# Performance work log

Measured on AMD Instinct MI355X. Metric: run time of the kernel, lower is better.

The kernel has to match this reference:

```python
import jax, jax.numpy as jnp
import numpy as np
import math

B, L, C_IN = 256, 128, 75
D_EMB = 128      # DataEmbedding d_model
D_MODEL = 126    # encoder d_model (= L-2 after ODConv valid conv k=3)
H = 6
D_HEAD = D_MODEL // H  # 21
D_FF = 2048
FACTOR = 5
K_NUM = 4        # ODConv kernel_num (default)
ATT_CH = 16      # max(int(128*0.0625), 16)
EPS = 1e-5


def _ln(x, g, b):
    m = x.mean(-1, keepdims=True)
    v = ((x - m) ** 2).mean(-1, keepdims=True)
    return (x - m) * jax.lax.rsqrt(v + EPS) * g + b


def _bn_eval(x, g, b):
    # eval-mode BatchNorm, running_mean=0 running_var=1
    return x * (g / np.sqrt(1.0 + EPS)) + b


def _conv1d(x, w, b=None):
    out = jax.lax.conv_general_dilated(x, w, (1,), 'VALID',
                                       dimension_numbers=('NCH', 'OIH', 'NCH'))
    if b is not None:
        out = out + b[None, :, None]
    return out


def _pos_embed(n, d):
    pos = np.arange(n)[:, None].astype(np.float32)
    div = np.exp(np.arange(0, d, 2).astype(np.float32) * (-math.log(10000.0) / d))
    pe = np.zeros((n, d), np.float32)
    pe[:, 0::2] = np.sin(pos * div)
    pe[:, 1::2] = np.cos(pos * div)
    return jnp.asarray(pe)


def _prob_attention(Q, K, V, key):
    # Informer ProbAttention, mask_flag=False. Q,K,V: [B,H,Lq,D]
    b, h, lq, d = Q.shape
    lk = K.shape[2]
    u_keys = min(FACTOR * int(np.ceil(np.log(lk))), lk)
    n_top = min(FACTOR * int(np.ceil(np.log(lq))), lq)
    idx = jax.random.randint(key, (lq, u_keys), 0, lk)     # sampled key ids per query
    K_s = K[:, :, idx, :]                                  # [B,H,Lq,u,D]
    qks = jnp.einsum('bhld,bhlud->bhlu', Q, K_s)
    M = qks.max(-1) - qks.sum(-1) / lk                     # sparsity measure
    _, top = jax.lax.top_k(M, n_top)                       # [B,H,n_top]
    Qr = jnp.take_along_axis(Q, top[..., None], axis=2)    # [B,H,n_top,D]
    scores = jnp.einsum('bhud,bhkd->bhuk', Qr, K) / np.sqrt(d).astype(np.float32)
    upd = jnp.einsum('bhuk,bhkd->bhud', jax.nn.softmax(scores, -1), V)
    ctx = jnp.broadcast_to(V.mean(2, keepdims=True), Q.shape)  # initial context
    bi = jnp.arange(b)[:, None, None]
    hi = jnp.arange(h)[None, :, None]
    return ctx.at[bi, hi, top].set(upd)


def _forward(x_enc, x_mark_enc, token_w, time_w, time_b,
             od_fc_w, od_bn_g, od_bn_b, od_ch_w, od_ch_b, od_fil_w, od_fil_b,
             od_sp_w, od_sp_b, od_ker_w, od_ker_b, od_weight,
             q_w, q_b, k_w, k_b, v_w, v_b, o_w, o_b,
             ffn1_w, ffn1_b, ffn2_w, ffn2_b, ln1_g, ln1_b, ln2_g, ln2_b,
             cl_w, cl_b, cl_bn_g, cl_bn_b, enc_ln_g, enc_ln_b, fc_w, fc_b):
    # ---- DataEmbedding (token circular conv + pos + timeF linear; dropout=eval) ----
    xt = jnp.pad(x_enc.transpose(0, 2, 1), ((0, 0), (0, 0), (1, 1)), mode='wrap')
    tok = _conv1d(xt, token_w).transpose(0, 2, 1)          # [B,L,128]
    emb = tok + _pos_embed(L, D_EMB)[None] + (x_mark_enc @ time_w + time_b)

    # ---- ODConv1d(128,128,k=3,pad=0) on [B,128,L] ----
    x = emb.transpose(0, 2, 1)                             # [B,128,L]
    gap = x.mean(-1)                                       # [B,128]
    a = jax.nn.relu(_bn_eval(gap @ od_fc_w, od_bn_g, od_bn_b))   # [B,16]
    ch_att = jax.nn.sigmoid(a @ od_ch_w + od_ch_b)         # [B,128]
    fil_att = jax.nn.sigmoid(a @ od_fil_w + od_fil_b)      # [B,128]
    sp_att = jax.nn.sigmoid(a @ od_sp_w + od_sp_b)         # [B,3]
    ker_att = jax.nn.softmax(a @ od_ker_w + od_ker_b, -1)  # [B,4]
    xc = x * ch_att[:, :, None]
    agg_w = jnp.einsum('bn,bj,noij->boij', ker_att, sp_att, od_weight)  # [B,128,128,3]
    lout = L - 2
    patches = jnp.stack([xc[:, :, j:j + lout] for j in range(3)], axis=2)  # [B,128,3,126]
    x = jnp.einsum('boij,bijt->bot', agg_w, patches) * fil_att[:, :, None]  # [B,128,126]
    # encoder reads this as (seq=128, d_model=126)

    key = jax.random.key(42)

    def enc_layer(xx, i):
        b, l, _ = xx.shape
        Q = (xx @ q_w[i] + q_b[i]).reshape(b, l, H, D_HEAD).transpose(0, 2, 1, 3)
        Kk = (xx @ k_w[i] + k_b[i]).reshape(b, l, H, D_HEAD).transpose(0, 2, 1, 3)
        Vv = (xx @ v_w[i] + v_b[i]).reshape(b, l, H, D_HEAD).transpose(0, 2, 1, 3)
        ctx = _prob_attention(Q, Kk, Vv, jax.random.fold_in(key, i))
        new_x = ctx.transpose(0, 2, 1, 3).reshape(b, l, D_MODEL) @ o_w[i] + o_b[i]
        xx = _ln(xx + new_x, ln1_g[i], ln1_b[i])
        y = jax.nn.gelu(xx @ ffn1_w[i] + ffn1_b[i], approximate=False)
        y = y @ ffn2_w[i] + ffn2_b[i]
        return _ln(xx + y, ln2_g[i], ln2_b[i])

    x = enc_layer(x, 0)
    # ConvLayer distilling: circular conv k3 + BN + ELU + maxpool(k3,s2,p1): 128 -> 64
    xt = jnp.pad(x.transpose(0, 2, 1), ((0, 0), (0, 0), (1, 1)), mode='wrap')
    xt = _conv1d(xt, cl_w, cl_b)
    xt = jax.nn.elu(_bn_eval(xt, cl_bn_g[None, :, None], cl_bn_b[None, :, None]))
    xt = jax.lax.reduce_window(xt, -jnp.inf, jax.lax.max, (1, 1, 3), (1, 1, 2),
                               [(0, 0), (0, 0), (1, 1)])
    x = xt.transpose(0, 2, 1)                              # [B,64,126]
    x = enc_layer(x, 1)
    x = _ln(x, enc_ln_g, enc_ln_b)

    out = x.transpose(0, 2, 1) @ fc_w + fc_b               # [B,126,1]
    return out.transpose(0, 2, 1)                          # [B,1,126]


def setup_inputs() -> dict:
    key = jax.random.key(0)
    it = iter(jax.random.split(key, 48))
    def rn(shape, s=0.05):
        return jax.random.normal(next(it), shape, dtype=jnp.float32) * s
    return {
        'x_enc': jax.random.normal(next(it), (B, L, C_IN), jnp.float32),
        'x_mark_enc': jax.random.uniform(next(it), (B, L, 3), jnp.float32, -0.5, 0.5),
        'token_w': rn((D_EMB, C_IN, 3), 0.1),
        'time_w': rn((3, D_EMB), 0.1), 'time_b': rn((D_EMB,)),
        'od_fc_w': rn((D_EMB, ATT_CH), 0.1),
        'od_bn_g': jnp.ones((ATT_CH,)), 'od_bn_b': jnp.zeros((ATT_CH,)),
        'od_ch_w': rn((ATT_CH, D_EMB), 0.1), 'od_ch_b': rn((D_EMB,)),
        'od_fil_w': rn((ATT_CH, D_EMB), 0.1), 'od_fil_b': rn((D_EMB,)),
        'od_sp_w': rn((ATT_CH, 3), 0.1), 'od_sp_b': rn((3,)),
        'od_ker_w': rn((ATT_CH, K_NUM), 0.1), 'od_ker_b': rn((K_NUM,)),
        'od_weight': rn((K_NUM, D_EMB, D_EMB, 3), 0.05),
        'q_w': rn((2, D_MODEL, D_MODEL)), 'q_b': rn((2, D_MODEL)),
        'k_w': rn((2, D_MODEL, D_MODEL)), 'k_b': rn((2, D_MODEL)),
        'v_w': rn((2, D_MODEL, D_MODEL)), 'v_b': rn((2, D_MODEL)),
        'o_w': rn((2, D_MODEL, D_MODEL)), 'o_b': rn((2, D_MODEL)),
        'ffn1_w': rn((2, D_MODEL, D_FF), 0.03), 'ffn1_b': rn((2, D_FF)),
        'ffn2_w': rn((2, D_FF, D_MODEL), 0.03), 'ffn2_b': rn((2, D_MODEL)),
        'ln1_g': jnp.ones((2, D_MODEL)), 'ln1_b': jnp.zeros((2, D_MODEL)),
        'ln2_g': jnp.ones((2, D_MODEL)), 'ln2_b': jnp.zeros((2, D_MODEL)),
        'cl_w': rn((D_MODEL, D_MODEL, 3), 0.05), 'cl_b': rn((D_MODEL,)),
        'cl_bn_g': jnp.ones((D_MODEL,)), 'cl_bn_b': jnp.zeros((D_MODEL,)),
        'enc_ln_g': jnp.ones((D_MODEL,)), 'enc_ln_b': jnp.zeros((D_MODEL,)),
        'fc_w': rn((L // 2, 1), 0.1), 'fc_b': rn((1,)),
    }


def reference(x_enc, x_mark_enc, token_w, time_w, time_b,
              od_fc_w, od_bn_g, od_bn_b, od_ch_w, od_ch_b, od_fil_w, od_fil_b,
              od_sp_w, od_sp_b, od_ker_w, od_ker_b, od_weight,
              q_w, q_b, k_w, k_b, v_w, v_b, o_w, o_b,
              ffn1_w, ffn1_b, ffn2_w, ffn2_b, ln1_g, ln1_b, ln2_g, ln2_b,
              cl_w, cl_b, cl_bn_g, cl_bn_b, enc_ln_g, enc_ln_b, fc_w, fc_b):
    return _forward(x_enc, x_mark_enc, token_w, time_w, time_b,
                    od_fc_w, od_bn_g, od_bn_b, od_ch_w, od_ch_b, od_fil_w, od_fil_b,
                    od_sp_w, od_sp_b, od_ker_w, od_ker_b, od_weight,
                    q_w, q_b, k_w, k_b, v_w, v_b, o_w, o_b,
                    ffn1_w, ffn1_b, ffn2_w, ffn2_b, ln1_g, ln1_b, ln2_g, ln2_b,
                    cl_w, cl_b, cl_bn_g, cl_bn_b, enc_ln_g, enc_ln_b, fc_w, fc_b)
```

## Files before the change

### kernel.cpp

```cpp
#include <hip/hip_runtime.h>
#include <math.h>

#define NB 256
#define DM 126
#define DE 128
#define NH 6
#define DHd 21
#define DFF 2048
#define CIN 75
#define L0 128
#define NTOP 25

#ifndef IDX_MODE
#define IDX_MODE 0
#endif

typedef const float* fp;
typedef unsigned short u16;
typedef short s8v __attribute__((ext_vector_type(8)));
typedef float f4v __attribute__((ext_vector_type(4)));

__device__ __forceinline__ u16 f2bf(float x){
  unsigned u = __float_as_uint(x);
  unsigned r = (u + 0x7FFFu + ((u >> 16) & 1u)) >> 16;
// ... 214 lines not shown
  __syncthreads();
  {
    f4v acc[2][8];
    #pragma unroll
    for (int m = 0; m < 2; m++)
      #pragma unroll
      for (int t = 0; t < 8; t++) acc[m][t] = z4;
    for (int ks = 0; ks < 8; ks++){
      s8v a0 = *reinterpret_cast<const s8v*>(sA + (mBase + l15)*264 + ks*32 + quad*8);
      s8v a1 = *reinterpret_cast<const s8v*>(sA + (mBase + 16 + l15)*264 + ks*32 + quad*8);
      const u16* wb = wemb + (size_t)l15*256 + ks*32 + quad*8;
      #pragma unroll
      for (int t = 0; t < 8; t++){
        s8v bfr = *reinterpret_cast<const s8v*>(wb + (size_t)t*16*256);
        acc[0][t] = __builtin_amdgcn_mfma_f32_16x16x32_bf16(a0, bfr, acc[0][t], 0, 0, 0);
        acc[1][t] = __builtin_amdgcn_mfma_f32_16x16x32_bf16(a1, bfr, acc[1][t], 0, 0, 0);
      }
    }
    float divc[8], tw0c[8], tw1c[8], tw2c[8], tbc[8];
    #pragma unroll
    for (int t = 0; t < 8; t++){
      int col = t*16 + l15;
      int i2 = col >> 1;
      divc[t] = __expf((float)(2*i2) * (-9.210340371976184f / 128.f));
      tw0c[t] = time_w[col]; tw1c[t] = time_w[128 + col]; tw2c[t] = time_w[256 + col];
      tbc[t] = time_b[col];
    }
    #pragma unroll
    for (int m = 0; m < 2; m++){
      #pragma unroll
      for (int r = 0; r < 4; r++){
        int row = mBase + m*16 + quad*4 + r;
        const float* mk = x_mark + ((size_t)b*L0 + row)*3;
        float m0v = mk[0], m1v = mk[1], m2v = mk[2];
        #pragma unroll
        for (int t = 0; t < 8; t++){
          int col = t*16 + l15;
          float ang = (float)row * divc[t];
          float pe = (col & 1) ? __cosf(ang) : __sinf(ang);
          float tm = m0v*tw0c[t] + m1v*tw1c[t] + m2v*tw2c[t] + tbc[t];
          sE[row*132 + col] = acc[m][t][r] + pe + tm;
        }
      }
    }
  }
  __syncthreads();
  {
    int col = tid & 127, half = tid >> 7;
    float s = 0.f;
    for (int r = 0; r < 64; r++) s += sE[(half*64 + r)*132 + col];
    red[tid] = s;
  }
  __syncthreads();
  if (tid < 128) gap[tid] = (red[tid] + red[tid + 128]) * (1.f/128.f);
  __syncthreads();
  if (tid < 16){
    float acc = 0.f;
    for (int e = 0; e < DE; e++) acc += gap[e]*fcw[e*16 + tid];
    acc = acc * (bng[tid] / sqrtf(1.f + 1e-5f)) + bnb[tid];
    aAct[tid] = fmaxf(acc, 0.f);
  }
  __syncthreads();
  if (tid < 128){
    float accc = 0.f, accf = 0.f;
    for (int c = 0; c < 16; c++){ accc += aAct[c]*chw[c*DE + tid]; accf += aAct[c]*filw[c*DE + tid]; }
    sch[tid]  = 1.f/(1.f + __expf(-(accc + chb[tid])));
    sfil[tid] = 1.f/(1.f + __expf(-(accf + filb[tid])));
  } else if (tid < 131){
    int t = tid - 128;
    float acc = 0.f;
    for (int c = 0; c < 16; c++) acc += aAct[c]*spw[c*3 + t];
    ssp[t] = 1.f/(1.f + __expf(-(acc + spb[t])));
  } else if (tid == 132){
    float v[4]; float mx = -1e30f;
    for (int n = 0; n < 4; n++){
      float acc = 0.f;
      for (int c = 0; c < 16; c++) acc += aAct[c]*kerw[c*4 + n];
      v[n] = acc + kerb[n]; mx = fmaxf(mx, v[n]);
    }
    float ss = 0.f;
    for (int n = 0; n < 4; n++){ v[n] = __expf(v[n]-mx); ss += v[n]; }
    for (int n = 0; n < 4; n++) sker[n] = v[n]/ss;
  }
  __syncthreads();
  for (int p = tid; p < 130*128; p += 256){
    int l = p >> 7, i = p & 127;
    float v = (l < 128) ? sE[l*132 + i]*sch[i] : 0.f;
    sXT[l*136 + i] = f2bf(v);
  }
  __syncthreads();
  {
    float kr0 = sker[0], kr1 = sker[1], kr2 = sker[2], kr3 = sker[3];
    float spq[3]; spq[0] = ssp[0]; spq[1] = ssp[1]; spq[2] = ssp[2];
    const float4* od4 = (const float4*)odw;
    for (int p4 = tid; p4 < 128*384/4; p4 += 256){
      float4 w0 = od4[p4];
      float4 w1 = od4[12288 + p4];
      float4 w2 = od4[24576 + p4];
      float4 w3 = od4[36864 + p4];
      float vv[4] = { kr0*w0.x + kr1*w1.x + kr2*w2.x + kr3*w3.x,
                      kr0*w0.y + kr1*w1.y + kr2*w2.y + kr3*w3.y,
                      kr0*w0.z + kr1*w1.z + kr2*w2.z + kr3*w3.z,
                      kr0*w0.w + kr1*w1.w + kr2*w2.w + kr3*w3.w };
      int e0 = p4*4;
      #pragma unroll
      for (int j = 0; j < 4; j++){
        int e = e0 + j;
        int o = e / 384, rem = e - o*384;
        int i = rem / 3, q = rem - i*3;
        sW[(q*128 + o)*136 + i] = f2bf(vv[j] * spq[q]);
      }
    }
  }
  __syncthreads();
  {
    f4v acc[2][8];
    #pragma unroll
    for (int m = 0; m < 2; m++)
      #pragma unroll
      for (int t = 0; t < 8; t++) acc[m][t] = z4;
    for (int q = 0; q < 3; q++){
      const u16* wq = sW + q*128*136;
      #pragma unroll
      for (int ks = 0; ks < 4; ks++){
        s8v a0 = *reinterpret_cast<const s8v*>(wq + (mBase + l15)*136 + ks*32 + quad*8);
        s8v a1 = *reinterpret_cast<const s8v*>(wq + (mBase + 16 + l15)*136 + ks*32 + quad*8);
        #pragma unroll
        for (int t = 0; t < 8; t++){
          s8v bfr = *reinterpret_cast<const s8v*>(sXT + (t*16 + l15 + q)*136 + ks*32 + quad*8);
          acc[0][t] = __builtin_amdgcn_mfma_f32_16x16x32_bf16(a0, bfr, acc[0][t], 0, 0, 0);
          acc[1][t] = __builtin_amdgcn_mfma_f32_16x16x32_bf16(a1, bfr, acc[1][t], 0, 0, 0);
        }
      }
    }
    #pragma unroll
    for (int t = 0; t < 8; t++){
      int tt = t*16 + l15;
      if (tt < DM){
        #pragma unroll
        for (int m = 0; m < 2; m++){
          #pragma unroll
          for (int r = 0; r < 4; r++){
            int o = mBase + m*16 + quad*4 + r;
            xout[((size_t)b*DE + o)*DM + tt] = sfil[o] * acc[m][t][r];
          }
        }
      }
    }
  }
}

__global__ __launch_bounds__(256) void k_qkv_mfma(const float* xin, const u16* wqkv,
                                                  const float* qkvb, float* qkv,
                                                  float* vt, int L, int lshift, int lmask){
  __shared__ __align__(16) u16 sX[64*136];
  const int tid = threadIdx.x;
  const int wave = tid >> 6, lane = tid & 63, quad = lane >> 4, l15 = lane & 15;
  const size_t rows0 = (size_t)blockIdx.x * 64;
  for (int p = tid; p < 64*128; p += 256){
    int r = p >> 7, c = p & 127;
    float v = (c < DM) ? xin[(rows0 + r)*DM + c] : 0.f;
    sX[r*136 + c] = f2bf(v);
  }
  __syncthreads();
  const f4v z4 = {0.f,0.f,0.f,0.f};
  f4v acc[24];
  #pragma unroll
  for (int t = 0; t < 24; t++) acc[t] = z4;
  const int m0 = wave * 16;
  #pragma unroll
  for (int ks = 0; ks < 4; ks++){
    s8v a = *reinterpret_cast<const s8v*>(sX + (m0 + l15)*136 + ks*32 + quad*8);
    const u16* wb = wqkv + (size_t)l15*128 + ks*32 + quad*8;
    #pragma unroll
    for (int t = 0; t < 24; t++){
      s8v b = *reinterpret_cast<const s8v*>(wb + (size_t)t*16*128);
      acc[t] = __builtin_amdgcn_mfma_f32_16x16x32_bf16(a, b, acc[t], 0, 0, 0);
    }
  }
  #pragma unroll
  for (int t = 0; t < 24; t++){
    int col = t*16 + l15;
    float bv = qkvb[col];
    if (col < 256){
      #pragma unroll
      for (int r = 0; r < 4; r++){
        int row = m0 + quad*4 + r;
        qkv[(rows0 + row)*256 + col] = acc[t][r] + bv;
      }
    } else {
      int c = col - 256;
      if (c < DM){
        int h = c / DHd, d = c - h*DHd;
        #pragma unroll
        for (int r = 0; r < 4; r++){
          int gr = (int)rows0 + m0 + quad*4 + r;
          int b = gr >> lshift, l = gr & lmask;
          vt[((size_t)(b*NH + h)*DHd + d)*L + l] = acc[t][r] + bv;
        }
      }
    }
  }
}

__global__ __launch_bounds__(128) void k_attn(const float* qkv, const float* vt,
                                              const int* idx, int L,
                                              int* posmap, float* vmean, float* upd){
  __shared__ __align__(16) float sK[2816];
  __shared__ int sTop[32];
  const int tid = threadIdx.x;
  const int wave = tid >> 6, lane = tid & 63, quad = lane >> 4, l15 = lane & 15;
  const int bh = blockIdx.x;
  const int b = bh / NH, h = bh - b*NH;
  float* sM = sK + 2688;
  u16* sPb = reinterpret_cast<u16*>(sK);
  const float* qbase = qkv + (size_t)(b*L)*256 + h*DHd;
  const float* vb = vt + (size_t)bh*DHd*L;
  const f4v z4 = {0.f,0.f,0.f,0.f};
  const int ntn = L >> 4;
  const int d0 = quad*8;
  const int mt = wave;

  for (int p = tid; p < L*DHd; p += 128){
    int l = p / DHd, d = p - l*DHd;
    sK[p] = qbase[(size_t)l*256 + 128 + d];
  }
  posmap[bh*L0 + tid] = -1;
  __syncthreads();
  if (tid < L){
    const int l = tid;
    const float* qg = qbase + (size_t)l*256;
    float qr[DHd];
    #pragma unroll
    for (int d = 0; d < DHd; d++) qr[d] = qg[d];
    float mx = -1e30f, sm = 0.f;
    #pragma unroll
    for (int u = 0; u < NTOP; u++){
      int kk = idx[l*NTOP + u];
      const float* kp = sK + kk*DHd;
      float acc = 0.f;
      #pragma unroll
      for (int d = 0; d < DHd; d++) acc += qr[d]*kp[d];
      mx = fmaxf(mx, acc); sm += acc;
    }
    sM[l] = mx - sm/(float)L;
  }
  __syncthreads();
  if (wave == 0){
    for (int it = 0; it < NTOP; it++){
      float bv = sM[lane]; int bi = lane;
      if (L == 128){
        float v1 = sM[lane + 64];
        if (v1 > bv){ bv = v1; bi = lane + 64; }
      }
      #pragma unroll
      for (int off = 32; off > 0; off >>= 1){
        float ov = __shfl_xor(bv, off);
        int   oi = __shfl_xor(bi, off);
        if (ov > bv || (ov == bv && oi < bi)){ bv = ov; bi = oi; }
      }
      if (lane == 0){
        sM[bi] = -1e30f;
        posmap[bh*L0 + bi] = it;
        sTop[it] = bi;
      }
    }
  }
  __syncthreads();

  s8v aq;
  {
    int uu = mt*16 + l15; if (uu >= NTOP) uu = 0;
    int r = sTop[uu];
    const float* qp = qbase + (size_t)r*256 + d0;
    #pragma unroll
    for (int j = 0; j < 8; j++) aq[j] = (short)f2bf(qp[j]);
  }
  f4v sc[8];
  for (int nt = 0; nt < ntn; nt++){
    const float* kp = sK + (size_t)(nt*16 + l15)*DHd + d0;
    s8v bb;
    #pragma unroll
    for (int j = 0; j < 8; j++) bb[j] = (d0 + j < DHd) ? (short)f2bf(kp[j]) : (short)0;
    sc[nt] = __builtin_amdgcn_mfma_f32_16x16x32_bf16(aq, bb, z4, 0, 0, 0);
  }
  __syncthreads();
  const float inv21 = 0.21821789023599236f;
  #pragma unroll
  for (int r4 = 0; r4 < 4; r4++){
    float mx = -1e30f;
    for (int nt = 0; nt < ntn; nt++) mx = fmaxf(mx, sc[nt][r4]*inv21);
    #pragma unroll
    for (int off = 1; off < 16; off <<= 1) mx = fmaxf(mx, __shfl_xor(mx, off));
    float e[8]; float ss = 0.f;
    for (int nt = 0; nt < ntn; nt++){ e[nt] = __expf(sc[nt][r4]*inv21 - mx); ss += e[nt]; }
    #pragma unroll
    for (int off = 1; off < 16; off <<= 1) ss += __shfl_xor(ss, off);
    float dn = 1.f / ss;
    int u = mt*16 + quad*4 + r4;
    for (int nt = 0; nt < ntn; nt++)
      sPb[u*136 + nt*16 + l15] = f2bf(e[nt]*dn);
  }
  if (wave == 1){
    u16 invL = f2bf(1.f/(float)L);
    for (int c = lane; c < L; c += 64) sPb[25*136 + c] = invL;
  }
  f4v pv[2];
  pv[0] = z4; pv[1] = z4;
  int kSteps = L >> 5;
  for (int ks = 0; ks < kSteps; ks++){
    #pragma unroll
    for (int nt = 0; nt < 2; nt++){
      int d = nt*16 + l15;
      s8v bb;
      if (d < DHd){
        const float* vp = vb + (size_t)d*L + ks*32 + d0;
        #pragma unroll
        for (int j = 0; j < 8; j++) bb[j] = (short)f2bf(vp[j]);
      } else {
        #pragma unroll
        for (int j = 0; j < 8; j++) bb[j] = (short)0;
      }
      s8v a = *reinterpret_cast<const s8v*>(sPb + (mt*16 + l15)*136 + ks*32 + d0);
      pv[nt] = __builtin_amdgcn_mfma_f32_16x16x32_bf16(a, bb, pv[nt], 0, 0, 0);
    }
  }
  #pragma unroll
  for (int nt = 0; nt < 2; nt++){
    #pragma unroll
    for (int r4 = 0; r4 < 4; r4++){
      int u = mt*16 + quad*4 + r4;
      int d = nt*16 + l15;
      if (d < DHd){
        if (u < NTOP)       upd[((size_t)bh*NTOP + u)*DHd + d] = pv[nt][r4];
        else if (u == NTOP) vmean[bh*DHd + d] = pv[nt][r4];
      }
    }
  }
}

__device__ __forceinline__ float gelu_fast(float x){
  float x2 = x*x;
  float u = x * __builtin_fmaf(0.10295128f, x2, 2.30212056f);
  u = fminf(u, 126.f);
#if __has_builtin(__builtin_amdgcn_exp2f)
  float t = __builtin_amdgcn_exp2f(u);
#else
  float t = __expf(u * 0.69314718056f);
#endif
  return x * t * __builtin_amdgcn_rcpf(t + 1.f);
}


__device__ __forceinline__ void stage_w1_p(const u16* w1t, int j, u16* buf, int p){
  int n = p >> 4, c = p & 15;
  int cg = c ^ (n & 7);
  gld_lds16(w1t + (((size_t)(j*64 + n)) << 7) + cg*8,
            buf + (size_t)((p >> 6) << 6)*8);
}
__device__ __forceinline__ void stage_w2_p(const u16* w2t, int j, u16* buf, int p){
  int n = p >> 3, c = p & 7;
  int cg = c ^ (n & 7);
  gld_lds16(w2t + (size_t)n*2048 + j*64 + cg*8,
            buf + (size_t)((p >> 6) << 6)*8);
}

__device__ __forceinline__ int yaddr(int row, int col){
  return row*64 + (((col >> 3) ^ (row & 7)) << 3) + (col & 7);
}

__device__ __forceinline__ void lgkm_barrier(){
  asm volatile("s_waitcnt lgkmcnt(0)" ::: "memory");
  __builtin_amdgcn_sched_barrier(0);
  __builtin_amdgcn_s_barrier();
  __builtin_amdgcn_sched_barrier(0);
}

template<int NT>
__global__ __launch_bounds__(NT) void k_ffn(const u16* w1t, const u16* w2t,
                                            fp b1, fp b2w, fp g, fp bb, int layer,
                                            const u16* wdist, fp e1, fp e2, fp e3, fp e4,
                                            const float* xres, const float* vmeanp,
                                            const int* posmapp, const float* updp,
                                            const u16* wo, fp obp, fp l1g, fp l1b,
                                            const u16* wqkv1, fp qb1, float* qkvout, float* vtout,
                                            float* out2){
  constexpr int ROWS = NT/8;
  constexpr int NMG  = NT/256;
  constexpr int SYG  = NMG*2048;
  constexpr int SP   = 1024/NT;
  constexpr int XMOFF = SYG + 4*8192;
  constexpr int TAILU = (NT == 1024) ? 128*392 : 0;
  constexpr int SMEMU = (XMOFF + ROWS*130*2) > TAILU ? (XMOFF + ROWS*130*2) : TAILU;
  __shared__ __align__(16) u16 smem[SMEMU];
  __shared__ float prs[2*ROWS];
  __shared__ float smean[ROWS], srstd[ROWS];
  u16* wA0 = smem + SYG;
  u16* wA1 = wA0 + 8192;
  u16* wB0 = wA1 + 8192;
  u16* wB1 = wB0 + 8192;
  const int tid  = threadIdx.x;
  const int wave = tid >> 6, lane = tid & 63, quad = lane >> 4, l15 = lane & 15;
  const int mg = wave >> 2, ng = wave & 3;
  const int rowb = mg * 32;
  u16* sYg = smem + mg*2048;
  const f4v z4 = {0.f, 0.f, 0.f, 0.f};
  float* xm = reinterpret_cast<float*>(smem + XMOFF);
  const int bb_ = blockIdx.x;

  {
    u16* sX = smem;
    for (int p = tid; p < ROWS*128; p += NT){
      int r = p >> 7, c = p & 127;
      float v = 0.f;
      if (c < DM){
        int h = c / DHd, d = c - h*DHd;
        int bh = bb_*NH + h;
        int pos = posmapp[bh*L0 + r];
        v = (pos >= 0) ? updp[((size_t)bh*NTOP + pos)*DHd + d] : vmeanp[bh*DHd + d];
      }
      sX[r*136 + c] = f2bf(v);
    }
    __syncthreads();
    constexpr int MT = ROWS/16;
    const int m0o = (wave % MT)*16;
    const int nb0 = (wave / MT)*4;
    const u16* wol = wo + (size_t)layer*16384;
    f4v oacc[4];
    oacc[0]=z4; oacc[1]=z4; oacc[2]=z4; oacc[3]=z4;
    #pragma unroll
    for (int ks = 0; ks < 4; ks++){
      s8v a = *reinterpret_cast<const s8v*>(sX + (m0o + l15)*136 + ks*32 + quad*8);
      const u16* wbp = wol + (size_t)l15*128 + ks*32 + quad*8;
      #pragma unroll
      for (int t = 0; t < 4; t++){
        s8v bfr = *reinterpret_cast<const s8v*>(wbp + (size_t)(nb0 + t)*16*128);
        oacc[t] = __builtin_amdgcn_mfma_f32_16x16x32_bf16(a, bfr, oacc[t], 0, 0, 0);
      }
    }
    __syncthreads();
    float* sOf = reinterpret_cast<float*>(smem);
    #pragma unroll
    for (int t = 0; t < 4; t++){
      int col = (nb0 + t)*16 + l15;
      #pragma unroll
      for (int r = 0; r < 4; r++)
        sOf[(m0o + quad*4 + r)*129 + col] = oacc[t][r];
    }
    __syncthreads();
    const float* obl = obp + (size_t)layer*DM;
    for (int p = tid; p < ROWS*DM; p += NT){
      int r = p / DM, c = p - r*DM;
      sOf[r*129 + c] += xres[((size_t)bb_*ROWS + r)*DM + c] + obl[c];
    }
    __syncthreads();
    if (tid < 2*ROWS){
      int row = tid >> 1, half = tid & 1;
      float s = 0.f;
      for (int c = half*63; c < half*63 + 63; c++) s += sOf[row*129 + c];
      prs[tid] = s;
    }
    __syncthreads();
    if (tid < 2*ROWS && (tid & 1) == 0) smean[tid>>1] = (prs[tid] + prs[tid+1]) / (float)DM;
    __syncthreads();
    if (tid < 2*ROWS){
      int row = tid >> 1, half = tid & 1;
      float mn = smean[row];
      float s = 0.f;
      for (int c = half*63; c < half*63 + 63; c++){ float d = sOf[row*129 + c] - mn; s += d*d; }
      prs[tid] = s;
    }
    __syncthreads();
    if (tid < 2*ROWS && (tid & 1) == 0) srstd[tid>>1] = rsqrtf((prs[tid] + prs[tid+1])/(float)DM + 1e-5f);
    __syncthreads();
    const float* l1gl = l1g + (size_t)layer*DM;
    const float* l1bl = l1b + (size_t)layer*DM;
    for (int p = tid; p < ROWS*DM; p += NT){
      int r = p / DM, c = p - r*DM;
      xm[r*130 + c] = (sOf[r*129 + c] - smean[r])*srstd[r]*l1gl[c] + l1bl[c];
    }
    __syncthreads();
  }

  s8v aX[2][4];
  #pragma unroll
  for (int mt = 0; mt < 2; mt++){
    #pragma unroll
    for (int ks = 0; ks < 4; ks++){
      #pragma unroll
      for (int jj2 = 0; jj2 < 8; jj2++){
        int c = ks*32 + quad*8 + jj2;
        float v = (c < DM) ? xm[(rowb + mt*16 + l15)*130 + c] : 0.f;
        aX[mt][ks][jj2] = (short)f2bf(v);
      }
    }
  }
  #pragma unroll
  for (int r = 0; r < SP; r++){
    stage_w1_p(w1t, 0, wA0, r*NT + tid);
    stage_w2_p(w2t, 0, wB0, r*NT + tid);
  }

  const float* b1l = b1 + (size_t)layer*DFF;
  f4v acc2[2][2];
  acc2[0][0]=z4; acc2[0][1]=z4; acc2[1][0]=z4; acc2[1][1]=z4;

  for (int j = 0; j < 32; j++){
    u16* wAcur = (j & 1) ? wA1 : wA0;
    u16* wAnxt = (j & 1) ? wA0 : wA1;
    u16* wBcur = (j & 1) ? wB1 : wB0;
    u16* wBnxt = (j & 1) ? wB0 : wB1;
    __syncthreads();
    if (j < 31){
      #pragma unroll
      for (int r = 0; r < SP; r++){
        stage_w1_p(w1t, j+1, wAnxt, r*NT + tid);
        stage_w2_p(w2t, j+1, wBnxt, r*NT + tid);
      }
    }
    f4v acc1[2];
    acc1[0] = z4; acc1[1] = z4;
    {
      int nloc = ng*16 + l15;
      #pragma unroll
      for (int ks = 0; ks < 4; ks++){
        int cg = (ks*4 + quad) ^ (nloc & 7);
        s8v b = *reinterpret_cast<const s8v*>(wAcur + nloc*128 + cg*8);
        acc1[0] = __builtin_amdgcn_mfma_f32_16x16x32_bf16(aX[0][ks], b, acc1[0], 0, 0, 0);
        acc1[1] = __builtin_amdgcn_mfma_f32_16x16x32_bf16(aX[1][ks], b, acc1[1], 0, 0, 0);
      }
    }
    {
      int col = ng*16 + l15;
      float bv = b1l[j*64 + col];
      #pragma unroll
      for (int mt = 0; mt < 2; mt++){
        float y0 = gelu_fast(acc1[mt][0] + bv);
        float y1 = gelu_fast(acc1[mt][1] + bv);
        float y2 = gelu_fast(acc1[mt][2] + bv);
        float y3 = gelu_fast(acc1[mt][3] + bv);
        unsigned p01 = cvt_pk_bf16(y0, y1);
        unsigned p23 = cvt_pk_bf16(y2, y3);
        int r0 = mt*16 + quad*4;
        sYg[yaddr(r0,     col)] = (u16)p01;
        sYg[yaddr(r0 + 1, col)] = (u16)(p01 >> 16);
        sYg[yaddr(r0 + 2, col)] = (u16)p23;
        sYg[yaddr(r0 + 3, col)] = (u16)(p23 >> 16);
      }
    }
    lgkm_barrier();
    #pragma unroll
    for (int ks2 = 0; ks2 < 2; ks2++){
      int ga = ((ks2*4 + quad) ^ (l15 & 7)) << 3;
      s8v a0 = *reinterpret_cast<const s8v*>(sYg + (l15)*64 + ga);
      s8v a1 = *reinterpret_cast<const s8v*>(sYg + (16 + l15)*64 + ga);
      #pragma unroll
      for (int t = 0; t < 2; t++){
        int nloc = ng*32 + t*16 + l15;
        int cg = (ks2*4 + quad) ^ (nloc & 7);
        s8v b = *reinterpret_cast<const s8v*>(wBcur + nloc*64 + cg*8);
        acc2[0][t] = __builtin_amdgcn_mfma_f32_16x16x32_bf16(a0, b, acc2[0][t], 0, 0, 0);
        acc2[1][t] = __builtin_amdgcn_mfma_f32_16x16x32_bf16(a1, b, acc2[1][t], 0, 0, 0);
      }
    }
  }

  __syncthreads();
  float* sO = reinterpret_cast<float*>(smem);
  #pragma unroll
  for (int mt = 0; mt < 2; mt++)
    #pragma unroll
    for (int t = 0; t < 2; t++)
      #pragma unroll
      for (int r = 0; r < 4; r++)
        sO[(rowb + mt*16 + quad*4 + r)*129 + ng*32 + t*16 + l15] = acc2[mt][t][r];
  __syncthreads();
  const float* b2l = b2w + (size_t)layer*DM;
  for (int p = tid; p < ROWS*DM; p += NT){
    int r = p / DM, c = p - r*DM;
    sO[r*129 + c] += b2l[c] + xm[r*130 + c];
  }
  __syncthreads();
  if (tid < 2*ROWS){
    int row = tid >> 1, half = tid & 1;
    float s = 0.f;
    for (int c = half*63; c < half*63 + 63; c++) s += sO[row*129 + c];
    prs[tid] = s;
  }
  __syncthreads();
  if (tid < 2*ROWS && (tid & 1) == 0) smean[tid>>1] = (prs[tid] + prs[tid+1]) / (float)DM;
  __syncthreads();
  if (tid < 2*ROWS){
    int row = tid >> 1, half = tid & 1;
    float mn = smean[row];
    float s = 0.f;
    for (int c = half*63; c < half*63 + 63; c++){ float d = sO[row*129 + c] - mn; s += d*d; }
    prs[tid] = s;
  }
  __syncthreads();
  if (tid < 2*ROWS && (tid & 1) == 0) srstd[tid>>1] = rsqrtf((prs[tid] + prs[tid+1])/(float)DM + 1e-5f);
  __syncthreads();
  const float* gl = g  + (size_t)layer*DM;
  const float* bl = bb + (size_t)layer*DM;

  if constexpr (NT == 1024){
    float rv[16];
    #pragma unroll
    for (int k = 0; k < 16; k++){
      int p = tid + k*1024;
      if (p < 128*DM){
        int r = p / DM, c = p - r*DM;
        rv[k] = (sO[r*129 + c] - smean[r])*srstd[r]*gl[c] + bl[c];
      } else rv[k] = 0.f;
    }
    __syncthreads();
    u16* sAd = smem;
    #pragma unroll
    for (int k = 0; k < 16; k++){
      int p = tid + k*1024;
      if (p < 128*DM){
        int r = p / DM, c = p - r*DM;
        u16 bv = f2bf(rv[k]);
        sAd[((r + 1) & 127)*392 + c] = bv;
        sAd[r*392 + 126 + c] = bv;
        sAd[((r + 127) & 127)*392 + 252 + c] = bv;
      }
    }
    if (tid < 768){ int row = tid / 6, c2 = tid - row*6; sAd[row*392 + 378 + c2] = 0; }
    __syncthreads();
    const int mrow  = (wave & 7) * 16;
    const int tbase = (wave >> 3) * 4;
    f4v dac[4];
    dac[0]=z4; dac[1]=z4; dac[2]=z4; dac[3]=z4;
    for (int ks = 0; ks < 12; ks++){
      s8v a = *reinterpret_cast<const s8v*>(sAd + (mrow + l15)*392 + ks*32 + quad*8);
      const u16* wbp = wdist + (size_t)l15*384 + ks*32 + quad*8;
      #pragma unroll
      for (int t = 0; t < 4; t++){
        s8v bfr = *reinterpret_cast<const s8v*>(wbp + (size_t)(tbase + t)*16*384);
        dac[t] = __builtin_amdgcn_mfma_f32_16x16x32_bf16(a, bfr, dac[t], 0, 0, 0);
      }
    }
    __syncthreads();
    float* zsh = reinterpret_cast<float*>(smem);
    const float bnscale = 1.f / sqrtf(1.f + 1e-5f);
    #pragma unroll
    for (int t = 0; t < 4; t++){
      int co = (tbase + t)*16 + l15;
      if (co < DM){
        float cb = e1[co];
        float gg = e2[co] * bnscale, bv = e3[co];
        #pragma unroll
        for (int r = 0; r < 4; r++){
          int row = mrow + quad*4 + r;
          float z = (dac[t][r] + cb)*gg + bv;
          z = (z > 0.f) ? z : (__expf(z) - 1.f);
          zsh[row*130 + co] = z;
        }
      }
    }
    __syncthreads();
    u16* sQ = smem + XMOFF;
    for (int p = tid; p < 64*128; p += 1024){
      int jj = p >> 7, co = p & 127;
      float best = 0.f;
      if (co < DM){
        best = zsh[(2*jj)*130 + co];
        if (jj > 0) best = fmaxf(best, zsh[(2*jj - 1)*130 + co]);
        best = fmaxf(best, zsh[(2*jj + 1)*130 + co]);
        out2[((size_t)bb_*64 + jj)*DM + co] = best;
      }
      sQ[jj*136 + co] = f2bf(best);
    }
    __syncthreads();
    {
      const int mq  = wave & 3;
      const int ngq = wave >> 2;
      f4v qa[6];
      #pragma unroll
      for (int t = 0; t < 6; t++) qa[t] = z4;
      #pragma unroll
      for (int ks = 0; ks < 4; ks++){
        s8v a = *reinterpret_cast<const s8v*>(sQ + (mq*16 + l15)*136 + ks*32 + quad*8);
        const u16* wbq = wqkv1 + (size_t)l15*128 + ks*32 + quad*8;
        #pragma unroll
        for (int t = 0; t < 6; t++){
          int nt = ngq*6 + t;
          s8v b = *reinterpret_cast<const s8v*>(wbq + (size_t)nt*16*128);
          qa[t] = __builtin_amdgcn_mfma_f32_16x16x32_bf16(a, b, qa[t], 0, 0, 0);
        }
      }
      #pragma unroll
      for (int t = 0; t < 6; t++){
        int col = (ngq*6 + t)*16 + l15;
        float bv = qb1[col];
        #pragma unroll
        for (int r = 0; r < 4; r++){
          int row = mq*16 + quad*4 + r;
          if (col < 256){
            qkvout[((size_t)bb_*64 + row)*256 + col] = qa[t][r] + bv;
          } else {
            int c = col - 256;
            if (c < DM){
              int h = c / DHd, d = c - h*DHd;
              vtout[((size_t)(bb_*NH + h)*DHd + d)*64 + row] = qa[t][r] + bv;
            }
          }
        }
      }
    }
  } else {
    for (int p = tid; p < ROWS*DM; p += NT){
      int r = p / DM, c = p - r*DM;
      sO[r*129 + c] = (sO[r*129 + c] - smean[r])*srstd[r]*gl[c] + bl[c];
    }
    __syncthreads();
    if (tid < 2*ROWS){
      int row = tid >> 1, half = tid & 1;
      float s = 0.f;
      for (int c = half*63; c < half*63 + 63; c++) s += sO[row*129 + c];
      prs[tid] = s;
    }
    __syncthreads();
    if (tid < 2*ROWS && (tid & 1) == 0) smean[tid>>1] = (prs[tid] + prs[tid+1]) / (float)DM;
    __syncthreads();
    if (tid < 2*ROWS){
      int row = tid >> 1, half = tid & 1;
      float mn = smean[row];
      float s = 0.f;
      for (int c = half*63; c < half*63 + 63; c++){ float d = sO[row*129 + c] - mn; s += d*d; }
      prs[tid] = s;
    }
    __syncthreads();
    if (tid < 2*ROWS && (tid & 1) == 0) srstd[tid>>1] = rsqrtf((prs[tid] + prs[tid+1])/(float)DM + 1e-5f);
    __syncthreads();
    if (tid < DM){
      float gv = e1[tid], bv2 = e2[tid];
      float acc = e4[0];
      for (int l = 0; l < 64; l++){
        float xn = (sO[l*129 + tid] - smean[l])*srstd[l]*gv + bv2;
        acc += xn * e3[l];
      }
      out2[(size_t)bb_*DM + tid] = acc;
    }
  }
}

extern "C" void kernel_launch(void* const* d_in, const int* in_sizes, int n_in,
                              void* d_out, int out_size, void* d_ws, size_t ws_size,
                              hipStream_t stream) {
  fp x_enc   = (fp)d_in[0];
  fp x_mark  = (fp)d_in[1];
  fp token_w = (fp)d_in[2];
  fp time_w  = (fp)d_in[3];
  fp time_b  = (fp)d_in[4];
  fp od_fc_w = (fp)d_in[5];
  fp od_bn_g = (fp)d_in[6];
  fp od_bn_b = (fp)d_in[7];
  fp od_ch_w = (fp)d_in[8];
  fp od_ch_b = (fp)d_in[9];
  fp od_fil_w= (fp)d_in[10];
  fp od_fil_b= (fp)d_in[11];
  fp od_sp_w = (fp)d_in[12];
  fp od_sp_b = (fp)d_in[13];
  fp od_ker_w= (fp)d_in[14];
  fp od_ker_b= (fp)d_in[15];
  fp od_wt   = (fp)d_in[16];
  fp q_w = (fp)d_in[17]; fp q_b = (fp)d_in[18];
  fp k_w = (fp)d_in[19]; fp k_b = (fp)d_in[20];
  fp v_w = (fp)d_in[21]; fp v_b = (fp)d_in[22];
  fp o_w = (fp)d_in[23]; fp o_b = (fp)d_in[24];
  fp f1w = (fp)d_in[25]; fp f1b = (fp)d_in[26];
  fp f2w = (fp)d_in[27]; fp f2b = (fp)d_in[28];
  fp ln1g= (fp)d_in[29]; fp ln1b= (fp)d_in[30];
  fp ln2g= (fp)d_in[31]; fp ln2b= (fp)d_in[32];
  fp cl_w= (fp)d_in[33]; fp cl_b= (fp)d_in[34];
  fp clbg= (fp)d_in[35]; fp clbb= (fp)d_in[36];
  fp elng= (fp)d_in[37]; fp elnb= (fp)d_in[38];
  fp fc_w= (fp)d_in[39]; fp fc_b= (fp)d_in[40];

  const size_t OFF_IDX0 = 0;
  const size_t OFF_IDX1 = OFF_IDX0 + 3200;
  const size_t OFF_CH   = OFF_IDX1 + 1600;
  const size_t OFF_FIL  = OFF_CH  + (size_t)NB*DE;
  const size_t OFF_SP   = OFF_FIL + (size_t)NB*DE;
  const size_t OFF_KER  = OFF_SP  + (size_t)NB*4;
  const size_t OFF_VM   = OFF_KER + (size_t)NB*4;
  const size_t OFF_POS  = OFF_VM  + (size_t)NB*NH*DHd;
  const size_t OFF_UPD  = OFF_POS + (size_t)NB*NH*L0;
  const size_t OFF_STOP = OFF_UPD + (size_t)NB*NH*NTOP*DHd;
  const size_t OFF_WTS  = (OFF_STOP + (size_t)NB*NH*NTOP + 255) & ~(size_t)255;
  const size_t WTS_FLOATS = (2*262144 + 2*262144 + 2*49152 + 2*16384 + 49152 + 32768)/2 + 2*384;
  const size_t OFF_BIG  = (OFF_WTS + WTS_FLOATS + 255) & ~(size_t)255;
  const size_t SBUF     = (size_t)NB*DE*L0;
  const size_t TOTAL    = OFF_BIG + 4*SBUF;

  if (ws_size < TOTAL*sizeof(float)){
    hipLaunchKernelGGL(k_zero, dim3((out_size+255)/256), dim3(256), 0, stream,
                       (float*)d_out, out_size);
    return;
  }

  float* ws = (float*)d_ws;
  int* idx0 = (int*)(ws + OFF_IDX0);
  int* idx1 = (int*)(ws + OFF_IDX1);
  float* vme = ws + OFF_VM;
  int* posm  = (int*)(ws + OFF_POS);
  float* updb= ws + OFF_UPD;
  u16* w1tb  = (u16*)(ws + OFF_WTS);
  u16* w2tb  = w1tb + 2*262144;
  u16* wqkvb = w2tb + 2*262144;
  u16* wob   = wqkvb + 2*49152;
  u16* wdistb= wob + 2*16384;
  u16* wembb = wdistb + 49152;
  float* qkvbias = (float*)(wembb + 32768);

  float* X    = ws + OFF_BIG;
  float* QKV  = X + SBUF;
  float* X2   = X + 2*SBUF;
  float* VT   = X + 3*SBUF;

  hipLaunchKernelGGL(k_prep, dim3(1092), dim3(256), 0, stream,
                     idx0, idx1, token_w, cl_w, q_w, q_b, k_w, k_b, v_w, v_b, o_w,
                     wembb, wdistb, wqkvb, wob, qkvbias,
                     f1w, f2w, w1tb, w2tb);
  hipLaunchKernelGGL(k_front, dim3(NB), dim3(256), 0, stream,
                     x_enc, x_mark, wembb, time_w, time_b,
                     od_fc_w, od_bn_g, od_bn_b, od_ch_w, od_ch_b, od_fil_w, od_fil_b,
                     od_sp_w, od_sp_b, od_ker_w, od_ker_b, od_wt, X);

  hipLaunchKernelGGL(k_qkv_mfma, dim3(NB*L0/64), dim3(256), 0, stream,
                     X, wqkvb, qkvbias, QKV, VT, 128, 7, 127);
  hipLaunchKernelGGL(k_attn, dim3(NB*NH), dim3(128), 0, stream,
                     QKV, VT, idx0, L0, posm, vme, updb);
  hipLaunchKernelGGL((k_ffn<1024>), dim3(NB), dim3(1024), 0, stream,
                     w1tb, w2tb, f1b, f2b, ln2g, ln2b, 0,
                     wdistb, cl_b, clbg, clbb, cl_b,
                     X, vme, posm, updb, wob, o_b, ln1g, ln1b,
                     wqkvb + 49152, qkvbias + 384, QKV, VT,
                     X2);

  hipLaunchKernelGGL(k_attn, dim3(NB*NH), dim3(128), 0, stream,
                     QKV, VT, idx1, 64, posm, vme, updb);
  hipLaunchKernelGGL((k_ffn<512>), dim3(256), dim3(512), 0, stream,
                     w1tb + 262144, w2tb + 262144, f1b, f2b, ln2g, ln2b, 1,
                     wdistb, elng, elnb, fc_w, fc_b,
                     X2, vme, posm, updb, wob, o_b, ln1g, ln1b,
                     wqkvb + 49152, qkvbias + 384, QKV, VT,
                     (float*)d_out);
  (void)in_sizes; (void)n_in; (void)out_size; (void)ws_size;
}
```

Measured before the change: 519.3 us.

## Store V-transpose and attention outputs as bf16; run layer-2 FFN with 1024 threads

The V-transpose buffer, the per-head context updates and the V means are now written in bf16 instead of fp32. This halves their global traffic and removes the fp32-to-bf16 conversions at the consumers. The FFN kernel is re-templated on row count and always launches 1024 threads. In the 64-row second layer, the extra waves only help stage weights and sit idle during the MFMA work, so the weight staging is spread over more threads. The cost is idle waves and a larger block, and attention outputs are rounded to bf16 earlier than before.

```diff
diff --git a/kernel.cpp b/kernel.cpp
--- a/kernel.cpp
+++ b/kernel.cpp
@@ -390,7 +390,7 @@
 
 __global__ __launch_bounds__(256) void k_qkv_mfma(const float* xin, const u16* wqkv,
                                                   const float* qkvb, float* qkv,
-                                                  float* vt, int L, int lshift, int lmask){
+                                                  u16* vt, int L, int lshift, int lmask){
   __shared__ __align__(16) u16 sX[64*136];
   const int tid = threadIdx.x;
   const int wave = tid >> 6, lane = tid & 63, quad = lane >> 4, l15 = lane & 15;
@@ -434,16 +434,16 @@
         for (int r = 0; r < 4; r++){
           int gr = (int)rows0 + m0 + quad*4 + r;
           int b = gr >> lshift, l = gr & lmask;
-          vt[((size_t)(b*NH + h)*DHd + d)*L + l] = acc[t][r] + bv;
+          vt[((size_t)(b*NH + h)*DHd + d)*L + l] = f2bf(acc[t][r] + bv);
         }
       }
     }
   }
 }
 
-__global__ __launch_bounds__(128) void k_attn(const float* qkv, const float* vt,
+__global__ __launch_bounds__(128) void k_attn(const float* qkv, const u16* vt,
                                               const int* idx, int L,
-                                              int* posmap, float* vmean, float* upd){
+                                              int* posmap, u16* vmean, u16* upd){
   __shared__ __align__(16) float sK[2816];
   __shared__ int sTop[32];
   const int tid = threadIdx.x;
@@ -453,7 +453,7 @@
   float* sM = sK + 2688;
   u16* sPb = reinterpret_cast<u16*>(sK);
   const float* qbase = qkv + (size_t)(b*L)*256 + h*DHd;
-  const float* vb = vt + (size_t)bh*DHd*L;
+  const u16* vb = vt + (size_t)bh*DHd*L;
   const f4v z4 = {0.f,0.f,0.f,0.f};
   const int ntn = L >> 4;
   const int d0 = quad*8;
@@ -552,9 +552,9 @@
       int d = nt*16 + l15;
       s8v bb;
       if (d < DHd){
-        const float* vp = vb + (size_t)d*L + ks*32 + d0;
-        #pragma unroll
-        for (int j = 0; j < 8; j++) bb[j] = (short)f2bf(vp[j]);
+        const u16* vp = vb + (size_t)d*L + ks*32 + d0;
+        #pragma unroll
+        for (int j = 0; j < 8; j++) bb[j] = (short)vp[j];
       } else {
         #pragma unroll
         for (int j = 0; j < 8; j++) bb[j] = (short)0;
@@ -570,8 +570,8 @@
       int u = mt*16 + quad*4 + r4;
       int d = nt*16 + l15;
       if (d < DHd){
-        if (u < NTOP)       upd[((size_t)bh*NTOP + u)*DHd + d] = pv[nt][r4];
-        else if (u == NTOP) vmean[bh*DHd + d] = pv[nt][r4];
+        if (u < NTOP)       upd[((size_t)bh*NTOP + u)*DHd + d] = f2bf(pv[nt][r4]);
+        else if (u == NTOP) vmean[bh*DHd + d] = f2bf(pv[nt][r4]);
       }
     }
   }
@@ -614,22 +614,23 @@
   __builtin_amdgcn_sched_barrier(0);
 }
 
-template<int NT>
-__global__ __launch_bounds__(NT) void k_ffn(const u16* w1t, const u16* w2t,
-                                            fp b1, fp b2w, fp g, fp bb, int layer,
-                                            const u16* wdist, fp e1, fp e2, fp e3, fp e4,
-                                            const float* xres, const float* vmeanp,
-                                            const int* posmapp, const float* updp,
-                                            const u16* wo, fp obp, fp l1g, fp l1b,
-                                            const u16* wqkv1, fp qb1, float* qkvout, float* vtout,
-                                            float* out2){
-  constexpr int ROWS = NT/8;
-  constexpr int NMG  = NT/256;
+template<int ROWS>
+__global__ __launch_bounds__(1024) void k_ffn(const u16* w1t, const u16* w2t,
+                                              fp b1, fp b2w, fp g, fp bb, int layer,
+                                              const u16* wdist, fp e1, fp e2, fp e3, fp e4,
+                                              const float* xres, const u16* vmeanp,
+                                              const int* posmapp, const u16* updp,
+                                              const u16* wo, fp obp, fp l1g, fp l1b,
+                                              const u16* wqkv1, fp qb1, float* qkvout, u16* vtout,
+                                              float* out2){
+  constexpr int NT   = 1024;
+  constexpr int NMG  = ROWS/32;
+  constexpr int NACT = NMG*4;
   constexpr int SYG  = NMG*2048;
-  constexpr int SP   = 1024/NT;
   constexpr int XMOFF = SYG + 4*8192;
-  constexpr int TAILU = (NT == 1024) ? 128*392 : 0;
-  constexpr int SMEMU = (XMOFF + ROWS*130*2) > TAILU ? (XMOFF + ROWS*130*2) : TAILU;
+  constexpr int TAILU = (ROWS == 128) ? 128*392 : 0;
+  constexpr int XMEND = XMOFF + ROWS*130*2;
+  constexpr int SMEMU = (XMEND > TAILU) ? XMEND : TAILU;
   __shared__ __align__(16) u16 smem[SMEMU];
   __shared__ float prs[2*ROWS];
   __shared__ float smean[ROWS], srstd[ROWS];
@@ -640,6 +641,7 @@
   const int tid  = threadIdx.x;
   const int wave = tid >> 6, lane = tid & 63, quad = lane >> 4, l15 = lane & 15;
   const int mg = wave >> 2, ng = wave & 3;
+  const bool act = (wave < NACT);
   const int rowb = mg * 32;
   u16* sYg = smem + mg*2048;
   const f4v z4 = {0.f, 0.f, 0.f, 0.f};
@@ -650,28 +652,31 @@
     u16* sX = smem;
     for (int p = tid; p < ROWS*128; p += NT){
       int r = p >> 7, c = p & 127;
-      float v = 0.f;
+      u16 v16 = 0;
       if (c < DM){
         int h = c / DHd, d = c - h*DHd;
         int bh = bb_*NH + h;
         int pos = posmapp[bh*L0 + r];
-        v = (pos >= 0) ? updp[((size_t)bh*NTOP + pos)*DHd + d] : vmeanp[bh*DHd + d];
-      }
-      sX[r*136 + c] = f2bf(v);
+        v16 = (pos >= 0) ? updp[((size_t)bh*NTOP + pos)*DHd + d] : vmeanp[bh*DHd + d];
+      }
+      sX[r*136 + c] = v16;
     }
     __syncthreads();
     constexpr int MT = ROWS/16;
+    constexpr int NGRP = 16/MT;
+    constexpr int NTILE = 8/NGRP;
     const int m0o = (wave % MT)*16;
-    const int nb0 = (wave / MT)*4;
+    const int nb0 = (wave / MT)*NTILE;
     const u16* wol = wo + (size_t)layer*16384;
-    f4v oacc[4];
-    oacc[0]=z4; oacc[1]=z4; oacc[2]=z4; oacc[3]=z4;
+    f4v oacc[NTILE];
+    #pragma unroll
+    for (int t = 0; t < NTILE; t++) oacc[t] = z4;
     #pragma unroll
     for (int ks = 0; ks < 4; ks++){
       s8v a = *reinterpret_cast<const s8v*>(sX + (m0o + l15)*136 + ks*32 + quad*8);
       const u16* wbp = wol + (size_t)l15*128 + ks*32 + quad*8;
       #pragma unroll
-      for (int t = 0; t < 4; t++){
+      for (int t = 0; t < NTILE; t++){
         s8v bfr = *reinterpret_cast<const s8v*>(wbp + (size_t)(nb0 + t)*16*128);
         oacc[t] = __builtin_amdgcn_mfma_f32_16x16x32_bf16(a, bfr, oacc[t], 0, 0, 0);
       }
@@ -679,7 +684,7 @@
     __syncthreads();
     float* sOf = reinterpret_cast<float*>(smem);
     #pragma unroll
-    for (int t = 0; t < 4; t++){
+    for (int t = 0; t < NTILE; t++){
       int col = (nb0 + t)*16 + l15;
       #pragma unroll
       for (int r = 0; r < 4; r++)
@@ -721,23 +726,22 @@
   }
 
   s8v aX[2][4];
-  #pragma unroll
-  for (int mt = 0; mt < 2; mt++){
-    #pragma unroll
-    for (int ks = 0; ks < 4; ks++){
-      #pragma unroll
-      for (int jj2 = 0; jj2 < 8; jj2++){
-        int c = ks*32 + quad*8 + jj2;
-        float v = (c < DM) ? xm[(rowb + mt*16 + l15)*130 + c] : 0.f;
-        aX[mt][ks][jj2] = (short)f2bf(v);
-      }
-    }
-  }
-  #pragma unroll
-  for (int r = 0; r < SP; r++){
-    stage_w1_p(w1t, 0, wA0, r*NT + tid);
-    stage_w2_p(w2t, 0, wB0, r*NT + tid);
-  }
+  if (act){
+    #pragma unroll
+    for (int mt = 0; mt < 2; mt++){
+      #pragma unroll
+      for (int ks = 0; ks < 4; ks++){
+        #pragma unroll
+        for (int jj2 = 0; jj2 < 8; jj2++){
+          int c = ks*32 + quad*8 + jj2;
+          float v = (c < DM) ? xm[(rowb + mt*16 + l15)*130 + c] : 0.f;
+          aX[mt][ks][jj2] = (short)f2bf(v);
+        }
+      }
+    }
+  }
+  stage_w1_p(w1t, 0, wA0, tid);
+  stage_w2_p(w2t, 0, wB0, tid);
 
   const float* b1l = b1 + (size_t)layer*DFF;
   f4v acc2[2][2];
@@ -750,68 +754,71 @@
     u16* wBnxt = (j & 1) ? wB0 : wB1;
     __syncthreads();
     if (j < 31){
-      #pragma unroll
-      for (int r = 0; r < SP; r++){
-        stage_w1_p(w1t, j+1, wAnxt, r*NT + tid);
-        stage_w2_p(w2t, j+1, wBnxt, r*NT + tid);
-      }
-    }
-    f4v acc1[2];
-    acc1[0] = z4; acc1[1] = z4;
-    {
-      int nloc = ng*16 + l15;
-      #pragma unroll
-      for (int ks = 0; ks < 4; ks++){
-        int cg = (ks*4 + quad) ^ (nloc & 7);
-        s8v b = *reinterpret_cast<const s8v*>(wAcur + nloc*128 + cg*8);
-        acc1[0] = __builtin_amdgcn_mfma_f32_16x16x32_bf16(aX[0][ks], b, acc1[0], 0, 0, 0);
-        acc1[1] = __builtin_amdgcn_mfma_f32_16x16x32_bf16(aX[1][ks], b, acc1[1], 0, 0, 0);
-      }
-    }
-    {
-      int col = ng*16 + l15;
-      float bv = b1l[j*64 + col];
-      #pragma unroll
-      for (int mt = 0; mt < 2; mt++){
-        float y0 = gelu_fast(acc1[mt][0] + bv);
-        float y1 = gelu_fast(acc1[mt][1] + bv);
-        float y2 = gelu_fast(acc1[mt][2] + bv);
-        float y3 = gelu_fast(acc1[mt][3] + bv);
-        unsigned p01 = cvt_pk_bf16(y0, y1);
-        unsigned p23 = cvt_pk_bf16(y2, y3);
-        int r0 = mt*16 + quad*4;
-        sYg[yaddr(r0,     col)] = (u16)p01;
-        sYg[yaddr(r0 + 1, col)] = (u16)(p01 >> 16);
-        sYg[yaddr(r0 + 2, col)] = (u16)p23;
-        sYg[yaddr(r0 + 3, col)] = (u16)(p23 >> 16);
+      stage_w1_p(w1t, j+1, wAnxt, tid);
+      stage_w2_p(w2t, j+1, wBnxt, tid);
+    }
+    if (act){
+      f4v acc1[2];
+      acc1[0] = z4; acc1[1] = z4;
+      {
+        int nloc = ng*16 + l15;
+        #pragma unroll
+        for (int ks = 0; ks < 4; ks++){
+          int cg = (ks*4 + quad) ^ (nloc & 7);
+          s8v b = *reinterpret_cast<const s8v*>(wAcur + nloc*128 + cg*8);
+          acc1[0] = __builtin_amdgcn_mfma_f32_16x16x32_bf16(aX[0][ks], b, acc1[0], 0, 0, 0);
+          acc1[1] = __builtin_amdgcn_mfma_f32_16x16x32_bf16(aX[1][ks], b, acc1[1], 0, 0, 0);
+        }
+      }
+      {
+        int col = ng*16 + l15;
+        float bv = b1l[j*64 + col];
+        #pragma unroll
+        for (int mt = 0; mt < 2; mt++){
+          float y0 = gelu_fast(acc1[mt][0] + bv);
+          float y1 = gelu_fast(acc1[mt][1] + bv);
+          float y2 = gelu_fast(acc1[mt][2] + bv);
+          float y3 = gelu_fast(acc1[mt][3] + bv);
+          unsigned p01 = cvt_pk_bf16(y0, y1);
+          unsigned p23 = cvt_pk_bf16(y2, y3);
+          int r0 = mt*16 + quad*4;
+          sYg[yaddr(r0,     col)] = (u16)p01;
+          sYg[yaddr(r0 + 1, col)] = (u16)(p01 >> 16);
+          sYg[yaddr(r0 + 2, col)] = (u16)p23;
+          sYg[yaddr(r0 + 3, col)] = (u16)(p23 >> 16);
+        }
       }
     }
     lgkm_barrier();
-    #pragma unroll
-    for (int ks2 = 0; ks2 < 2; ks2++){
-      int ga = ((ks2*4 + quad) ^ (l15 & 7)) << 3;
-      s8v a0 = *reinterpret_cast<const s8v*>(sYg + (l15)*64 + ga);
-      s8v a1 = *reinterpret_cast<const s8v*>(sYg + (16 + l15)*64 + ga);
-      #pragma unroll
-      for (int t = 0; t < 2; t++){
-        int nloc = ng*32 + t*16 + l15;
-        int cg = (ks2*4 + quad) ^ (nloc & 7);
-        s8v b = *reinterpret_cast<const s8v*>(wBcur + nloc*64 + cg*8);
-        acc2[0][t] = __builtin_amdgcn_mfma_f32_16x16x32_bf16(a0, b, acc2[0][t], 0, 0, 0);
-        acc2[1][t] = __builtin_amdgcn_mfma_f32_16x16x32_bf16(a1, b, acc2[1][t], 0, 0, 0);
+    if (act){
+      #pragma unroll
+      for (int ks2 = 0; ks2 < 2; ks2++){
+        int ga = ((ks2*4 + quad) ^ (l15 & 7)) << 3;
+        s8v a0 = *reinterpret_cast<const s8v*>(sYg + (l15)*64 + ga);
+        s8v a1 = *reinterpret_cast<const s8v*>(sYg + (16 + l15)*64 + ga);
+        #pragma unroll
+        for (int t = 0; t < 2; t++){
+          int nloc = ng*32 + t*16 + l15;
+          int cg = (ks2*4 + quad) ^ (nloc & 7);
+          s8v b = *reinterpret_cast<const s8v*>(wBcur + nloc*64 + cg*8);
+          acc2[0][t] = __builtin_amdgcn_mfma_f32_16x16x32_bf16(a0, b, acc2[0][t], 0, 0, 0);
+          acc2[1][t] = __builtin_amdgcn_mfma_f32_16x16x32_bf16(a1, b, acc2[1][t], 0, 0, 0);
+        }
       }
     }
   }
 
   __syncthreads();
   float* sO = reinterpret_cast<float*>(smem);
-  #pragma unroll
-  for (int mt = 0; mt < 2; mt++)
-    #pragma unroll
-    for (int t = 0; t < 2; t++)
-      #pragma unroll
-      for (int r = 0; r < 4; r++)
-        sO[(rowb + mt*16 + quad*4 + r)*129 + ng*32 + t*16 + l15] = acc2[mt][t][r];
+  if (act){
+    #pragma unroll
+    for (int mt = 0; mt < 2; mt++)
+      #pragma unroll
+      for (int t = 0; t < 2; t++)
+        #pragma unroll
+        for (int r = 0; r < 4; r++)
+          sO[(rowb + mt*16 + quad*4 + r)*129 + ng*32 + t*16 + l15] = acc2[mt][t][r];
+  }
   __syncthreads();
   const float* b2l = b2w + (size_t)layer*DM;
   for (int p = tid; p < ROWS*DM; p += NT){
@@ -841,7 +848,7 @@
   const float* gl = g  + (size_t)layer*DM;
   const float* bl = bb + (size_t)layer*DM;
 
-  if constexpr (NT == 1024){
+  if constexpr (ROWS == 128){
     float rv[16];
     #pragma unroll
     for (int k = 0; k < 16; k++){
@@ -941,7 +948,7 @@
             int c = col - 256;
             if (c < DM){
               int h = c / DHd, d = c - h*DHd;
-              vtout[((size_t)(bb_*NH + h)*DHd + d)*64 + row] = qa[t][r] + bv;
+              vtout[((size_t)(bb_*NH + h)*DHd + d)*64 + row] = f2bf(qa[t][r] + bv);
             }
           }
         }
@@ -1042,9 +1049,9 @@
   float* ws = (float*)d_ws;
   int* idx0 = (int*)(ws + OFF_IDX0);
   int* idx1 = (int*)(ws + OFF_IDX1);
-  float* vme = ws + OFF_VM;
+  u16* vme  = (u16*)(ws + OFF_VM);
   int* posm  = (int*)(ws + OFF_POS);
-  float* updb= ws + OFF_UPD;
+  u16* updb  = (u16*)(ws + OFF_UPD);
   u16* w1tb  = (u16*)(ws + OFF_WTS);
   u16* w2tb  = w1tb + 2*262144;
   u16* wqkvb = w2tb + 2*262144;
@@ -1056,7 +1063,7 @@
   float* X    = ws + OFF_BIG;
   float* QKV  = X + SBUF;
   float* X2   = X + 2*SBUF;
-  float* VT   = X + 3*SBUF;
+  u16*   VTb  = (u16*)(X + 3*SBUF);
 
   hipLaunchKernelGGL(k_prep, dim3(1092), dim3(256), 0, stream,
                      idx0, idx1, token_w, cl_w, q_w, q_b, k_w, k_b, v_w, v_b, o_w,
@@ -1068,23 +1075,23 @@
                      od_sp_w, od_sp_b, od_ker_w, od_ker_b, od_wt, X);
 
   hipLaunchKernelGGL(k_qkv_mfma, dim3(NB*L0/64), dim3(256), 0, stream,
-                     X, wqkvb, qkvbias, QKV, VT, 128, 7, 127);
+                     X, wqkvb, qkvbias, QKV, VTb, 128, 7, 127);
   hipLaunchKernelGGL(k_attn, dim3(NB*NH), dim3(128), 0, stream,
-                     QKV, VT, idx0, L0, posm, vme, updb);
-  hipLaunchKernelGGL((k_ffn<1024>), dim3(NB), dim3(1024), 0, stream,
+                     QKV, VTb, idx0, L0, posm, vme, updb);
+  hipLaunchKernelGGL((k_ffn<128>), dim3(NB), dim3(1024), 0, stream,
                      w1tb, w2tb, f1b, f2b, ln2g, ln2b, 0,
                      wdistb, cl_b, clbg, clbb, cl_b,
                      X, vme, posm, updb, wob, o_b, ln1g, ln1b,
-                     wqkvb + 49152, qkvbias + 384, QKV, VT,
+                     wqkvb + 49152, qkvbias + 384, QKV, VTb,
                      X2);
 
   hipLaunchKernelGGL(k_attn, dim3(NB*NH), dim3(128), 0, stream,
-                     QKV, VT, idx1, 64, posm, vme, updb);
-  hipLaunchKernelGGL((k_ffn<512>), dim3(256), dim3(512), 0, stream,
+                     QKV, VTb, idx1, 64, posm, vme, updb);
+  hipLaunchKernelGGL((k_ffn<64>), dim3(256), dim3(1024), 0, stream,
                      w1tb + 262144, w2tb + 262144, f1b, f2b, ln2g, ln2b, 1,
                      wdistb, elng, elnb, fc_w, fc_b,
                      X2, vme, posm, updb, wob, o_b, ln1g, ln1b,
-                     wqkvb + 49152, qkvbias + 384, QKV, VT,
+                     wqkvb + 49152, qkvbias + 384, QKV, VTb,
                      (float*)d_out);
   (void)in_sizes; (void)n_in; (void)out_size; (void)ws_size;
 }
```

Result: faster. 506.5 us (-2.5%).
